# Kernel tuning notes

Measured on AMD Instinct MI355X. Metric: run time of the kernel, lower is better.

The kernel has to match this reference:

```python
import jax, jax.numpy as jnp
import numpy as np

B, F, N = 128, 256, 2000

def setup_inputs() -> dict:
    key = jax.random.key(0)
    ks = jax.random.split(key, 10)
    s = 0.05
    return {
        'nfeature': jax.random.normal(ks[0], (B, F, N, 1), jnp.float32),
        'last_current': jax.random.randint(ks[1], (B, 2), 0, N, jnp.int32),
        'Wg': jax.random.normal(ks[2], (F, F), jnp.float32) * s,
        'bg': jax.random.normal(ks[3], (F,), jnp.float32) * s,
        'Wnode': jax.random.normal(ks[4], (3 * F, F), jnp.float32) * s,
        'bnode': jax.random.normal(ks[5], (3 * F,), jnp.float32) * s,
        'Wlc': jax.random.normal(ks[6], (F, 2 * F), jnp.float32) * s,
        'blc': jax.random.normal(ks[7], (F,), jnp.float32) * s,
        'Wproj': jax.random.normal(ks[8], (F, F), jnp.float32) * s,
        'bproj': jax.random.normal(ks[9], (F,), jnp.float32) * s,
    }

def reference(nfeature, last_current, Wg, bg, Wnode, bnode, Wlc, blc, Wproj, bproj):
    # nfeature: [B, F, N, 1]
    x = nfeature[..., 0]                                  # [B, F, N]
    f = x.shape[1]
    scale = 1.0 / jnp.sqrt(jnp.asarray(f, x.dtype))
    # global fixed query: max over nodes then Linear
    glb = jnp.max(x, axis=2)                              # [B, F]
    Q = glb @ Wg.T + bg                                   # [B, F]
    # node embeddings via 1x1 conv == channel GEMM, split into K, V, logit_K
    kvl = jnp.einsum('bfn,gf->bgn', x, Wnode) + bnode[None, :, None]  # [B, 3F, N]
    K, V, Klog = jnp.split(kvl, 3, axis=1)                # each [B, F, N]
    # gather last/current city features
    lc = jnp.take_along_axis(x, last_current[:, None, :], axis=2)     # [B, F, 2]
    context = jnp.concatenate([lc[:, :, 0], lc[:, :, 1]], axis=1)     # [B, 2F]
    cQ = context @ Wlc.T + blc + Q                        # [B, F]
    # attention: single query over N keys
    ucj = jnp.einsum('bf,bfn->bn', cQ, K) * scale         # [B, N]
    attn = jax.nn.softmax(ucj, axis=1)
    nc = jnp.einsum('bn,bfn->bf', attn, V)                # [B, F]
    nc = nc @ Wproj.T + bproj                             # [B, F]
    logits = jnp.einsum('bf,bfn->bn', nc, Klog) * scale   # [B, N]
    return jnp.tanh(logits) * 10.0
```

## Files before the change

kernel.cpp:

```cpp
#include <hip/hip_runtime.h>
#include <hip/hip_fp16.h>
#include <math.h>

#define BB 128
#define FF 256
#define NN 2000
#define SWA 16
#define SCA 128
#define SWL 8
#define SCL 256

typedef float f32x4 __attribute__((ext_vector_type(4)));
union H8 { f32x4 v; __half2 h[4]; };

__device__ __forceinline__ float sel8(f32x4 a, f32x4 b, int e) {
    float v;
    switch (e) {
        case 0: v = a.x; break; case 1: v = a.y; break;
        case 2: v = a.z; break; case 3: v = a.w; break;
        case 4: v = b.x; break; case 5: v = b.y; break;
        case 6: v = b.z; break; default: v = b.w; break;
    }
    return v;
}

__device__ __forceinline__ float dot4(f32x4 a, f32x4 b) {
    float s = a.x * b.x;
    s = fmaf(a.y, b.y, s);
    s = fmaf(a.z, b.z, s);
    s = fmaf(a.w, b.w, s);
    return s;
}

__global__ __launch_bounds__(256) void k_convmax(const float* __restrict__ x,
                                                 const int* __restrict__ lc,
                                                 __half* __restrict__ xh,
                                                 float* __restrict__ glb,
                                                 float* __restrict__ xg) {
    int row  = (blockIdx.x << 2) | (threadIdx.x >> 6);
    int lane = threadIdx.x & 63;
    int b    = row >> 8;
    const int c0 = lc[2 * b], c1 = lc[2 * b + 1];
    const int i0 = c0 >> 3, e0 = c0 & 7;
    const int i1 = c1 >> 3, e1 = c1 & 7;
    const f32x4* src = (const f32x4*)(x + (size_t)row * NN);
    f32x4*       dst = (f32x4*)(xh + (size_t)row * NN);
    float m = -INFINITY;
    for (int i = lane; i < 250; i += 64) {
        f32x4 a = __builtin_nontemporal_load(src + 2 * i);
        f32x4 q = __builtin_nontemporal_load(src + 2 * i + 1);
        m = fmaxf(m, fmaxf(fmaxf(a.x, a.y), fmaxf(a.z, a.w)));
        m = fmaxf(m, fmaxf(fmaxf(q.x, q.y), fmaxf(q.z, q.w)));
        if (i == i0) xg[row * 2]     = sel8(a, q, e0);
        if (i == i1) xg[row * 2 + 1] = sel8(a, q, e1);
        H8 o;
        o.h[0] = __floats2half2_rn(a.x, a.y);
        o.h[1] = __floats2half2_rn(a.z, a.w);
        o.h[2] = __floats2half2_rn(q.x, q.y);
        o.h[3] = __floats2half2_rn(q.z, q.w);
        dst[i] = o.v;
    }
#pragma unroll
    for (int off = 32; off; off >>= 1) m = fmaxf(m, __shfl_xor(m, off));
    if (!lane) glb[row] = m;
}

__global__ __launch_bounds__(256) void k_prep(
    const float* __restrict__ xg, const float* __restrict__ glb,
    const float* __restrict__ Wg, const float* __restrict__ bg,
    const float* __restrict__ Wnode, const float* __restrict__ bnode,
    const float* __restrict__ Wlc, const float* __restrict__ blc,
    float* __restrict__ cK, float* __restrict__ cK0)
{
    int b = blockIdx.x, tid = threadIdx.x, w = tid >> 6, lane = tid & 63;
    __shared__ float s_glb[FF], s_ctx[2 * FF], s_cQ[FF], s_bias[FF], s_red[FF];
    s_glb[tid] = glb[b * FF + tid];
    float2 g2 = ((const float2*)xg)[b * FF + tid];
    s_ctx[tid]      = g2.x;
    s_ctx[FF + tid] = g2.y;
    s_bias[tid] = bg[tid] + blc[tid];
    __syncthreads();

    f32x4 gv  = *(const f32x4*)&s_glb[lane << 2];
    f32x4 c0v = *(const f32x4*)&s_ctx[lane << 3];
    f32x4 c1v = *(const f32x4*)&s_ctx[(lane << 3) + 4];

    for (int k = 0; k < 64; k += 4) {
        float p0, p1, p2, p3;
        {
            int fb = (w << 6) + k;
            f32x4 wg0 = *(const f32x4*)(Wg + (size_t)fb * FF + (lane << 2));
            f32x4 wg1 = *(const f32x4*)(Wg + (size_t)(fb + 1) * FF + (lane << 2));
            f32x4 wg2 = *(const f32x4*)(Wg + (size_t)(fb + 2) * FF + (lane << 2));
            f32x4 wg3 = *(const f32x4*)(Wg + (size_t)(fb + 3) * FF + (lane << 2));
            f32x4 wa0 = *(const f32x4*)(Wlc + (size_t)fb * 2 * FF + (lane << 3));
            f32x4 wb0 = *(const f32x4*)(Wlc + (size_t)fb * 2 * FF + (lane << 3) + 4);
            f32x4 wa1 = *(const f32x4*)(Wlc + (size_t)(fb + 1) * 2 * FF + (lane << 3));
            f32x4 wb1 = *(const f32x4*)(Wlc + (size_t)(fb + 1) * 2 * FF + (lane << 3) + 4);
            f32x4 wa2 = *(const f32x4*)(Wlc + (size_t)(fb + 2) * 2 * FF + (lane << 3));
            f32x4 wb2 = *(const f32x4*)(Wlc + (size_t)(fb + 2) * 2 * FF + (lane << 3) + 4);
            f32x4 wa3 = *(const f32x4*)(Wlc + (size_t)(fb + 3) * 2 * FF + (lane << 3));
            f32x4 wb3 = *(const f32x4*)(Wlc + (size_t)(fb + 3) * 2 * FF + (lane << 3) + 4);
            p0 = dot4(wg0, gv) + dot4(wa0, c0v) + dot4(wb0, c1v);
            p1 = dot4(wg1, gv) + dot4(wa1, c0v) + dot4(wb1, c1v);
            p2 = dot4(wg2, gv) + dot4(wa2, c0v) + dot4(wb2, c1v);
            p3 = dot4(wg3, gv) + dot4(wa3, c0v) + dot4(wb3, c1v);
        }
#pragma unroll
        for (int off = 32; off; off >>= 1) {
            p0 += __shfl_xor(p0, off);
            p1 += __shfl_xor(p1, off);
            p2 += __shfl_xor(p2, off);
            p3 += __shfl_xor(p3, off);
        }
        if (lane == 0) {
            int fb = (w << 6) + k;
            s_cQ[fb]     = p0 + s_bias[fb];
            s_cQ[fb + 1] = p1 + s_bias[fb + 1];
            s_cQ[fb + 2] = p2 + s_bias[fb + 2];
            s_cQ[fb + 3] = p3 + s_bias[fb + 3];
        }
    }
    __syncthreads();

    {
        float a0 = 0, a1 = 0, a2 = 0, a3 = 0, a4 = 0, a5 = 0, a6 = 0, a7 = 0;
        for (int g = 0; g < FF; g += 8) {
            float w0 = Wnode[(size_t)(g + 0) * FF + tid];
            float w1 = Wnode[(size_t)(g + 1) * FF + tid];
            float w2 = Wnode[(size_t)(g + 2) * FF + tid];
            float w3 = Wnode[(size_t)(g + 3) * FF + tid];
            float w4 = Wnode[(size_t)(g + 4) * FF + tid];
            float w5 = Wnode[(size_t)(g + 5) * FF + tid];
            float w6 = Wnode[(size_t)(g + 6) * FF + tid];
            float w7 = Wnode[(size_t)(g + 7) * FF + tid];
            a0 = fmaf(s_cQ[g + 0], w0, a0); a1 = fmaf(s_cQ[g + 1], w1, a1);
            a2 = fmaf(s_cQ[g + 2], w2, a2); a3 = fmaf(s_cQ[g + 3], w3, a3);
            a4 = fmaf(s_cQ[g + 4], w4, a4); a5 = fmaf(s_cQ[g + 5], w5, a5);
            a6 = fmaf(s_cQ[g + 6], w6, a6); a7 = fmaf(s_cQ[g + 7], w7, a7);
        }
        cK[b * FF + tid] = ((a0 + a1) + (a2 + a3)) + ((a4 + a5) + (a6 + a7));
    }
    s_red[tid] = s_cQ[tid] * bnode[tid];
    __syncthreads();
    for (int s = 128; s > 0; s >>= 1) {
        if (tid < s) s_red[tid] += s_red[tid + s];
        __syncthreads();
    }
    if (tid == 0) cK0[b] = s_red[0];
}

__global__ __launch_bounds__(512) void k_attn(
    const __half* __restrict__ xh,
    const float* __restrict__ cK, const float* __restrict__ cK0,
    float* __restrict__ y_part, float* __restrict__ m_part,
    float* __restrict__ s_part)
{
    int b = blockIdx.x >> 4, st = blockIdx.x & 15;
    int tid = threadIdx.x, w = tid >> 6, lane = tid & 63;
    int par = lane >> 4, chunk = lane & 15;
    __shared__ float tbuf[8][512];
    __shared__ float s_u[8][SCA];
    __shared__ float s_p[SCA];
    __shared__ float s_cK[FF];
    __shared__ float s_red[8], s_red2[8];
    if (tid < FF) s_cK[tid] = cK[b * FF + tid];
    __syncthreads();

    int colbase = (st << 7) + (chunk << 3);
    bool cvalid = colbase < NN;
    const __half* base = xh + ((size_t)(b * FF) + (w << 5) + par) * NN + colbase;
    const f32x4 zero = {0.f, 0.f, 0.f, 0.f};

    f32x4 hv[8];
#pragma unroll
    for (int r = 0; r < 8; ++r)
        hv[r] = cvalid ? *(const f32x4*)(base + (size_t)(r << 2) * NN) : zero;

    float uc0 = 0, uc1 = 0, uc2 = 0, uc3 = 0, uc4 = 0, uc5 = 0, uc6 = 0, uc7 = 0;
#pragma unroll
    for (int r = 0; r < 8; ++r) {
        int row = (w << 5) + (r << 2) + par;
        H8 u; u.v = hv[r];
        float c = s_cK[row];
        float2 q0 = __half22float2(u.h[0]);
        float2 q1 = __half22float2(u.h[1]);
        float2 q2 = __half22float2(u.h[2]);
        float2 q3 = __half22float2(u.h[3]);
        uc0 = fmaf(c, q0.x, uc0); uc1 = fmaf(c, q0.y, uc1);
        uc2 = fmaf(c, q1.x, uc2); uc3 = fmaf(c, q1.y, uc3);
        uc4 = fmaf(c, q2.x, uc4); uc5 = fmaf(c, q2.y, uc5);
        uc6 = fmaf(c, q3.x, uc6); uc7 = fmaf(c, q3.y, uc7);
    }
    uc0 += __shfl_xor(uc0, 16); uc0 += __shfl_xor(uc0, 32);
    uc1 += __shfl_xor(uc1, 16); uc1 += __shfl_xor(uc1, 32);
    uc2 += __shfl_xor(uc2, 16); uc2 += __shfl_xor(uc2, 32);
    uc3 += __shfl_xor(uc3, 16); uc3 += __shfl_xor(uc3, 32);
    uc4 += __shfl_xor(uc4, 16); uc4 += __shfl_xor(uc4, 32);
    uc5 += __shfl_xor(uc5, 16); uc5 += __shfl_xor(uc5, 32);
    uc6 += __shfl_xor(uc6, 16); uc6 += __shfl_xor(uc6, 32);
    uc7 += __shfl_xor(uc7, 16); uc7 += __shfl_xor(uc7, 32);
    if (par == 0) {
        f32x4 v0 = {uc0, uc1, uc2, uc3}, v1 = {uc4, uc5, uc6, uc7};
        *(f32x4*)&s_u[w][chunk << 3]       = v0;
        *(f32x4*)&s_u[w][(chunk << 3) + 4] = v1;
    }
    __syncthreads();

    const float scale = 0.0625f;
    float uu = -INFINITY;
    if (tid < SCA) {
        int col = (st << 7) + tid;
        if (col < NN) {
            float usum = 0.f;
#pragma unroll
            for (int ww = 0; ww < 8; ++ww) usum += s_u[ww][tid];
            uu = (usum + cK0[b]) * scale;
        }
    }
    float m = uu;
#pragma unroll
    for (int off = 32; off; off >>= 1) m = fmaxf(m, __shfl_xor(m, off));
    if (!lane && w < 2) s_red[w] = m;
    __syncthreads();
    float M = fmaxf(s_red[0], s_red[1]);
    float e = (uu > -INFINITY) ? __expf(uu - M) : 0.f;
    if (tid < SCA) s_p[tid] = e;
    float ssum = e;
#pragma unroll
    for (int off = 32; off; off >>= 1) ssum += __shfl_xor(ssum, off);
    if (!lane && w < 2) s_red2[w] = ssum;
    __syncthreads();
    if (!tid) {
        m_part[(b << 4) + st] = M;
        s_part[(b << 4) + st] = s_red2[0] + s_red2[1];
    }

    f32x4 pv0 = *(const f32x4*)&s_p[chunk << 3];
    f32x4 pv1 = *(const f32x4*)&s_p[(chunk << 3) + 4];
#pragma unroll
    for (int r = 0; r < 8; ++r) {
        H8 u; u.v = hv[r];
        float2 q0 = __half22float2(u.h[0]);
        float2 q1 = __half22float2(u.h[1]);
        float2 q2 = __half22float2(u.h[2]);
        float2 q3 = __half22float2(u.h[3]);
        float a = 0.f;
        a = fmaf(pv0.x, q0.x, a); a = fmaf(pv0.y, q0.y, a);
        a = fmaf(pv0.z, q1.x, a); a = fmaf(pv0.w, q1.y, a);
        a = fmaf(pv1.x, q2.x, a); a = fmaf(pv1.y, q2.y, a);
        a = fmaf(pv1.z, q3.x, a); a = fmaf(pv1.w, q3.y, a);
        tbuf[w][(((r << 2) + par) << 4) + chunk] = a;
    }
    {
        int row = tid >> 1, half = tid & 1;
        const float* srcp = &tbuf[row >> 5][((row & 31) << 4) + (half << 3)];
        f32x4 a0 = *(const f32x4*)srcp;
        f32x4 a1 = *(const f32x4*)(srcp + 4);
        float sm = ((a0.x + a0.y) + (a0.z + a0.w)) + ((a1.x + a1.y) + (a1.z + a1.w));
        sm += __shfl_xor(sm, 1);
        if (!half) y_part[(size_t)((b << 4) + st) * FF + row] = sm;
    }
}

__global__ __launch_bounds__(256) void k_dense(
    const float* __restrict__ y_part, const float* __restrict__ m_part,
    const float* __restrict__ s_part,
    const float* __restrict__ Wnode, const float* __restrict__ bnode,
    const float* __restrict__ Wproj, const float* __restrict__ bproj,
    float* __restrict__ cL, float* __restrict__ cL0)
{
    int b = blockIdx.x, tid = threadIdx.x, w = tid >> 6, lane = tid & 63;
    __shared__ float s_y[FF], s_v[FF], s_n[FF], s_b1[FF], s_b2[FF], s_red[FF];

    s_b1[tid] = bnode[FF + tid];
    s_b2[tid] = bproj[tid];
    float M = -INFINITY;
#pragma unroll
    for (int s = 0; s < 16; ++s) M = fmaxf(M, m_part[(b << 4) + s]);
    float S = 0.f, wgt[16];
#pragma unroll
    for (int s = 0; s < 16; ++s) {
        wgt[s] = __expf(m_part[(b << 4) + s] - M);
        S = fmaf(wgt[s], s_part[(b << 4) + s], S);
    }
    float invS = 1.0f / S;
    float acc = 0.f;
#pragma unroll
    for (int s = 0; s < 16; ++s)
        acc = fmaf(wgt[s], y_part[(size_t)((b << 4) + s) * FF + tid], acc);
    s_y[tid] = acc * invS;
    __syncthreads();

    {
        f32x4 yv = *(const f32x4*)&s_y[lane << 2];
        for (int k = 0; k < 64; k += 4) {
            int fb = (w << 6) + k;
            f32x4 w0 = *(const f32x4*)(Wnode + (size_t)(FF + fb) * FF + (lane << 2));
            f32x4 w1 = *(const f32x4*)(Wnode + (size_t)(FF + fb + 1) * FF + (lane << 2));
            f32x4 w2 = *(const f32x4*)(Wnode + (size_t)(FF + fb + 2) * FF + (lane << 2));
            f32x4 w3 = *(const f32x4*)(Wnode + (size_t)(FF + fb + 3) * FF + (lane << 2));
            float p0 = dot4(w0, yv), p1 = dot4(w1, yv), p2 = dot4(w2, yv), p3 = dot4(w3, yv);
#pragma unroll
            for (int off = 32; off; off >>= 1) {
                p0 += __shfl_xor(p0, off);
                p1 += __shfl_xor(p1, off);
                p2 += __shfl_xor(p2, off);
                p3 += __shfl_xor(p3, off);
            }
            if (lane == 0) {
                s_v[fb]     = p0 + s_b1[fb];
                s_v[fb + 1] = p1 + s_b1[fb + 1];
                s_v[fb + 2] = p2 + s_b1[fb + 2];
                s_v[fb + 3] = p3 + s_b1[fb + 3];
            }
        }
    }
    __syncthreads();
    {
        f32x4 vv = *(const f32x4*)&s_v[lane << 2];
        for (int k = 0; k < 64; k += 4) {
            int fb = (w << 6) + k;
            f32x4 w0 = *(const f32x4*)(Wproj + (size_t)fb * FF + (lane << 2));
            f32x4 w1 = *(const f32x4*)(Wproj + (size_t)(fb + 1) * FF + (lane << 2));
            f32x4 w2 = *(const f32x4*)(Wproj + (size_t)(fb + 2) * FF + (lane << 2));
            f32x4 w3 = *(const f32x4*)(Wproj + (size_t)(fb + 3) * FF + (lane << 2));
            float p0 = dot4(w0, vv), p1 = dot4(w1, vv), p2 = dot4(w2, vv), p3 = dot4(w3, vv);
#pragma unroll
            for (int off = 32; off; off >>= 1) {
                p0 += __shfl_xor(p0, off);
                p1 += __shfl_xor(p1, off);
                p2 += __shfl_xor(p2, off);
                p3 += __shfl_xor(p3, off);
            }
            if (lane == 0) {
                s_n[fb]     = p0 + s_b2[fb];
                s_n[fb + 1] = p1 + s_b2[fb + 1];
                s_n[fb + 2] = p2 + s_b2[fb + 2];
                s_n[fb + 3] = p3 + s_b2[fb + 3];
            }
        }
    }
    __syncthreads();
    {
        float a0 = 0, a1 = 0, a2 = 0, a3 = 0, a4 = 0, a5 = 0, a6 = 0, a7 = 0;
        for (int g = 0; g < FF; g += 8) {
            float w0 = Wnode[(size_t)(2 * FF + g + 0) * FF + tid];
            float w1 = Wnode[(size_t)(2 * FF + g + 1) * FF + tid];
            float w2 = Wnode[(size_t)(2 * FF + g + 2) * FF + tid];
            float w3 = Wnode[(size_t)(2 * FF + g + 3) * FF + tid];
            float w4 = Wnode[(size_t)(2 * FF + g + 4) * FF + tid];
            float w5 = Wnode[(size_t)(2 * FF + g + 5) * FF + tid];
            float w6 = Wnode[(size_t)(2 * FF + g + 6) * FF + tid];
            float w7 = Wnode[(size_t)(2 * FF + g + 7) * FF + tid];
            a0 = fmaf(s_n[g + 0], w0, a0); a1 = fmaf(s_n[g + 1], w1, a1);
            a2 = fmaf(s_n[g + 2], w2, a2); a3 = fmaf(s_n[g + 3], w3, a3);
            a4 = fmaf(s_n[g + 4], w4, a4); a5 = fmaf(s_n[g + 5], w5, a5);
            a6 = fmaf(s_n[g + 6], w6, a6); a7 = fmaf(s_n[g + 7], w7, a7);
        }
        cL[b * FF + tid] = ((a0 + a1) + (a2 + a3)) + ((a4 + a5) + (a6 + a7));
    }
    s_red[tid] = s_n[tid] * bnode[2 * FF + tid];
    __syncthreads();
    for (int s = 128; s > 0; s >>= 1) {
        if (tid < s) s_red[tid] += s_red[tid + s];
        __syncthreads();
    }
    if (tid == 0) cL0[b] = s_red[0];
}

__global__ __launch_bounds__(512) void k_logits(const __half* __restrict__ xh,
                                                const float* __restrict__ cL,
                                                const float* __restrict__ cL0,
                                                float* __restrict__ out)
{
    int b = blockIdx.x >> 3, st = blockIdx.x & 7;
    int tid = threadIdx.x, w = tid >> 6, lane = tid & 63;
    int par = lane >> 5, chunk = lane & 31;
    __shared__ float s_cL[FF];
    __shared__ float s_acc[8][SCL];
    if (tid < FF) s_cL[tid] = cL[b * FF + tid];
    __syncthreads();

    int colbase = (st << 8) + (chunk << 3);
    bool cvalid = colbase < NN;
    const __half* base = xh + ((size_t)(b * FF) + (w << 5) + par) * NN + colbase;
    const f32x4 zero = {0.f, 0.f, 0.f, 0.f};
    float up0 = 0, up1 = 0, up2 = 0, up3 = 0, up4 = 0, up5 = 0, up6 = 0, up7 = 0;
#pragma unroll
    for (int h = 0; h < 2; ++h) {
        f32x4 hv[8];
#pragma unroll
        for (int r = 0; r < 8; ++r)
            hv[r] = cvalid ? *(const f32x4*)(base + (size_t)((h << 4) + (r << 1)) * NN) : zero;
#pragma unroll
        for (int r = 0; r < 8; ++r) {
            int row = (w << 5) + par + (h << 4) + (r << 1);
            H8 u; u.v = hv[r];
            float c = s_cL[row];
            float2 q0 = __half22float2(u.h[0]);
            float2 q1 = __half22float2(u.h[1]);
            float2 q2 = __half22float2(u.h[2]);
            float2 q3 = __half22float2(u.h[3]);
            up0 = fmaf(c, q0.x, up0); up1 = fmaf(c, q0.y, up1);
            up2 = fmaf(c, q1.x, up2); up3 = fmaf(c, q1.y, up3);
            up4 = fmaf(c, q2.x, up4); up5 = fmaf(c, q2.y, up5);
            up6 = fmaf(c, q3.x, up6); up7 = fmaf(c, q3.y, up7);
        }
    }
    up0 += __shfl_xor(up0, 32); up1 += __shfl_xor(up1, 32);
    up2 += __shfl_xor(up2, 32); up3 += __shfl_xor(up3, 32);
    up4 += __shfl_xor(up4, 32); up5 += __shfl_xor(up5, 32);
    up6 += __shfl_xor(up6, 32); up7 += __shfl_xor(up7, 32);
    if (!par) {
        f32x4 v0 = {up0, up1, up2, up3}, v1 = {up4, up5, up6, up7};
        *(f32x4*)&s_acc[w][chunk << 3]       = v0;
        *(f32x4*)&s_acc[w][(chunk << 3) + 4] = v1;
    }
    __syncthreads();
    if (tid < SCL) {
        int col = (st << 8) + tid;
        if (col < NN) {
            float t = 0.f;
#pragma unroll
            for (int ww = 0; ww < 8; ++ww) t += s_acc[ww][tid];
            out[(size_t)b * NN + col] = tanhf((t + cL0[b]) * 0.0625f) * 10.f;
        }
    }
}

extern "C" void kernel_launch(void* const* d_in, const int* in_sizes, int n_in,
                              void* d_out, int out_size, void* d_ws, size_t ws_size,
                              hipStream_t stream) {
    const float* x     = (const float*)d_in[0];
    const int*   lc    = (const int*)d_in[1];
    const float* Wg    = (const float*)d_in[2];
    const float* bg    = (const float*)d_in[3];
    const float* Wnode = (const float*)d_in[4];
    const float* bnode = (const float*)d_in[5];
    const float* Wlc   = (const float*)d_in[6];
    const float* blc   = (const float*)d_in[7];
    const float* Wproj = (const float*)d_in[8];
    const float* bproj = (const float*)d_in[9];
    float* out = (float*)d_out;

    float* ws     = (float*)d_ws;
    float* glb    = ws + 0;
    float* xg     = ws + 32768;
    float* cK     = ws + 98304;
    float* cK0    = ws + 131072;
    float* m_part = ws + 132096;
    float* s_part = ws + 134144;
    float* cL     = ws + 136192;
    float* cL0    = ws + 168960;
    float* y_part = ws + 169984;
    __half* xh    = (__half*)(ws + (2 << 20));

    k_convmax<<<BB * FF / 4, 256, 0, stream>>>(x, lc, xh, glb, xg);
    k_prep   <<<BB, 256, 0, stream>>>(xg, glb, Wg, bg, Wnode, bnode, Wlc, blc, cK, cK0);
    k_attn   <<<BB * SWA, 512, 0, stream>>>(xh, cK, cK0, y_part, m_part, s_part);
    k_dense  <<<BB, 256, 0, stream>>>(y_part, m_part, s_part, Wnode, bnode, Wproj, bproj, cL, cL0);
    k_logits <<<BB * SWL, 512, 0, stream>>>(xh, cL, cL0, out);
}
```

Measured before the change: 177.5 us.

## Tile the fp16 copy of x into contiguous per-slice blocks for attn and logits

```diff
diff --git a/kernel.cpp b/kernel.cpp
--- a/kernel.cpp
+++ b/kernel.cpp
@@ -7,8 +7,6 @@
 #define NN 2000
 #define SWA 16
 #define SCA 128
-#define SWL 8
-#define SCL 256
 
 typedef float f32x4 __attribute__((ext_vector_type(4)));
 union H8 { f32x4 v; __half2 h[4]; };
@@ -40,11 +38,12 @@
     int row  = (blockIdx.x << 2) | (threadIdx.x >> 6);
     int lane = threadIdx.x & 63;
     int b    = row >> 8;
+    int f    = row & 255;
     const int c0 = lc[2 * b], c1 = lc[2 * b + 1];
     const int i0 = c0 >> 3, e0 = c0 & 7;
     const int i1 = c1 >> 3, e1 = c1 & 7;
     const f32x4* src = (const f32x4*)(x + (size_t)row * NN);
-    f32x4*       dst = (f32x4*)(xh + (size_t)row * NN);
+    __half* trow = xh + ((size_t)(b << 4) * 256 + f) * 128;
     float m = -INFINITY;
     for (int i = lane; i < 250; i += 64) {
         f32x4 a = __builtin_nontemporal_load(src + 2 * i);
@@ -58,7 +57,12 @@
         o.h[1] = __floats2half2_rn(a.z, a.w);
         o.h[2] = __floats2half2_rn(q.x, q.y);
         o.h[3] = __floats2half2_rn(q.z, q.w);
-        dst[i] = o.v;
+        *(f32x4*)(trow + (size_t)(i >> 4) * 32768 + ((i & 15) << 3)) = o.v;
+    }
+    if (lane < 6) {
+        int i = 250 + lane;
+        f32x4 z = {0.f, 0.f, 0.f, 0.f};
+        *(f32x4*)(trow + (size_t)15 * 32768 + ((i & 15) << 3)) = z;
     }
 #pragma unroll
     for (int off = 32; off; off >>= 1) m = fmaxf(m, __shfl_xor(m, off));
@@ -167,15 +171,12 @@
     if (tid < FF) s_cK[tid] = cK[b * FF + tid];
     __syncthreads();
 
-    int colbase = (st << 7) + (chunk << 3);
-    bool cvalid = colbase < NN;
-    const __half* base = xh + ((size_t)(b * FF) + (w << 5) + par) * NN + colbase;
-    const f32x4 zero = {0.f, 0.f, 0.f, 0.f};
+    const __half* base = xh + ((size_t)((b << 4) + st) * 256 + (w << 5) + par) * 128 + (chunk << 3);
 
     f32x4 hv[8];
 #pragma unroll
     for (int r = 0; r < 8; ++r)
-        hv[r] = cvalid ? *(const f32x4*)(base + (size_t)(r << 2) * NN) : zero;
+        hv[r] = *(const f32x4*)(base + (size_t)(r << 9));
 
     float uc0 = 0, uc1 = 0, uc2 = 0, uc3 = 0, uc4 = 0, uc5 = 0, uc6 = 0, uc7 = 0;
 #pragma unroll
@@ -374,52 +375,51 @@
                                                 const float* __restrict__ cL0,
                                                 float* __restrict__ out)
 {
-    int b = blockIdx.x >> 3, st = blockIdx.x & 7;
+    int b = blockIdx.x >> 4, st = blockIdx.x & 15;
     int tid = threadIdx.x, w = tid >> 6, lane = tid & 63;
-    int par = lane >> 5, chunk = lane & 31;
+    int par = lane >> 4, chunk = lane & 15;
     __shared__ float s_cL[FF];
-    __shared__ float s_acc[8][SCL];
+    __shared__ float s_acc[8][SCA];
     if (tid < FF) s_cL[tid] = cL[b * FF + tid];
     __syncthreads();
 
-    int colbase = (st << 8) + (chunk << 3);
-    bool cvalid = colbase < NN;
-    const __half* base = xh + ((size_t)(b * FF) + (w << 5) + par) * NN + colbase;
-    const f32x4 zero = {0.f, 0.f, 0.f, 0.f};
-    float up0 = 0, up1 = 0, up2 = 0, up3 = 0, up4 = 0, up5 = 0, up6 = 0, up7 = 0;
-#pragma unroll
-    for (int h = 0; h < 2; ++h) {
-        f32x4 hv[8];
-#pragma unroll
-        for (int r = 0; r < 8; ++r)
-            hv[r] = cvalid ? *(const f32x4*)(base + (size_t)((h << 4) + (r << 1)) * NN) : zero;
-#pragma unroll
-        for (int r = 0; r < 8; ++r) {
-            int row = (w << 5) + par + (h << 4) + (r << 1);
-            H8 u; u.v = hv[r];
-            float c = s_cL[row];
-            float2 q0 = __half22float2(u.h[0]);
-            float2 q1 = __half22float2(u.h[1]);
-            float2 q2 = __half22float2(u.h[2]);
-            float2 q3 = __half22float2(u.h[3]);
-            up0 = fmaf(c, q0.x, up0); up1 = fmaf(c, q0.y, up1);
-            up2 = fmaf(c, q1.x, up2); up3 = fmaf(c, q1.y, up3);
-            up4 = fmaf(c, q2.x, up4); up5 = fmaf(c, q2.y, up5);
-            up6 = fmaf(c, q3.x, up6); up7 = fmaf(c, q3.y, up7);
-        }
-    }
-    up0 += __shfl_xor(up0, 32); up1 += __shfl_xor(up1, 32);
-    up2 += __shfl_xor(up2, 32); up3 += __shfl_xor(up3, 32);
-    up4 += __shfl_xor(up4, 32); up5 += __shfl_xor(up5, 32);
-    up6 += __shfl_xor(up6, 32); up7 += __shfl_xor(up7, 32);
-    if (!par) {
-        f32x4 v0 = {up0, up1, up2, up3}, v1 = {up4, up5, up6, up7};
+    const __half* base = xh + ((size_t)((b << 4) + st) * 256 + (w << 5) + par) * 128 + (chunk << 3);
+    f32x4 hv[8];
+#pragma unroll
+    for (int r = 0; r < 8; ++r)
+        hv[r] = *(const f32x4*)(base + (size_t)(r << 9));
+
+    float uc0 = 0, uc1 = 0, uc2 = 0, uc3 = 0, uc4 = 0, uc5 = 0, uc6 = 0, uc7 = 0;
+#pragma unroll
+    for (int r = 0; r < 8; ++r) {
+        int row = (w << 5) + (r << 2) + par;
+        H8 u; u.v = hv[r];
+        float c = s_cL[row];
+        float2 q0 = __half22float2(u.h[0]);
+        float2 q1 = __half22float2(u.h[1]);
+        float2 q2 = __half22float2(u.h[2]);
+        float2 q3 = __half22float2(u.h[3]);
+        uc0 = fmaf(c, q0.x, uc0); uc1 = fmaf(c, q0.y, uc1);
+        uc2 = fmaf(c, q1.x, uc2); uc3 = fmaf(c, q1.y, uc3);
+        uc4 = fmaf(c, q2.x, uc4); uc5 = fmaf(c, q2.y, uc5);
+        uc6 = fmaf(c, q3.x, uc6); uc7 = fmaf(c, q3.y, uc7);
+    }
+    uc0 += __shfl_xor(uc0, 16); uc0 += __shfl_xor(uc0, 32);
+    uc1 += __shfl_xor(uc1, 16); uc1 += __shfl_xor(uc1, 32);
+    uc2 += __shfl_xor(uc2, 16); uc2 += __shfl_xor(uc2, 32);
+    uc3 += __shfl_xor(uc3, 16); uc3 += __shfl_xor(uc3, 32);
+    uc4 += __shfl_xor(uc4, 16); uc4 += __shfl_xor(uc4, 32);
+    uc5 += __shfl_xor(uc5, 16); uc5 += __shfl_xor(uc5, 32);
+    uc6 += __shfl_xor(uc6, 16); uc6 += __shfl_xor(uc6, 32);
+    uc7 += __shfl_xor(uc7, 16); uc7 += __shfl_xor(uc7, 32);
+    if (par == 0) {
+        f32x4 v0 = {uc0, uc1, uc2, uc3}, v1 = {uc4, uc5, uc6, uc7};
         *(f32x4*)&s_acc[w][chunk << 3]       = v0;
         *(f32x4*)&s_acc[w][(chunk << 3) + 4] = v1;
     }
     __syncthreads();
-    if (tid < SCL) {
-        int col = (st << 8) + tid;
+    if (tid < SCA) {
+        int col = (st << 7) + tid;
         if (col < NN) {
             float t = 0.f;
 #pragma unroll
@@ -460,5 +460,5 @@
     k_prep   <<<BB, 256, 0, stream>>>(xg, glb, Wg, bg, Wnode, bnode, Wlc, blc, cK, cK0);
     k_attn   <<<BB * SWA, 512, 0, stream>>>(xh, cK, cK0, y_part, m_part, s_part);
     k_dense  <<<BB, 256, 0, stream>>>(y_part, m_part, s_part, Wnode, bnode, Wproj, bproj, cL, cL0);
-    k_logits <<<BB * SWL, 512, 0, stream>>>(xh, cL, cL0, out);
-}
+    k_logits <<<BB * SWA, 512, 0, stream>>>(xh, cL, cL0, out);
+}
```

Result: faster. 165.5 us (-6.8%).
